# Optimization experiments

Hardware: AMD Instinct MI355X
Metric: run time of the kernel (lower is better)

## Reference

```python
import jax, jax.numpy as jnp
import numpy as np

EMB_DIM = 64
NUM_HEADS = 8
BATCH = 32
SEQ = 1024


def setup_inputs() -> dict:
    key = jax.random.key(0)
    k1, k2, k3 = jax.random.split(key, 3)
    hidden = EMB_DIM * NUM_HEADS  # 512
    x = jax.random.normal(k1, (BATCH, SEQ, EMB_DIM), dtype=jnp.float32)
    # torch Linear weights, stored here as (in, out) for x @ W
    w_qkv = jax.random.normal(k2, (EMB_DIM, 3 * hidden), dtype=jnp.float32) * (1.0 / np.sqrt(EMB_DIM))
    b_qkv = jnp.zeros((3 * hidden,), dtype=jnp.float32)
    w_proj = jax.random.normal(k3, (hidden, EMB_DIM), dtype=jnp.float32) * (1.0 / np.sqrt(hidden))
    b_proj = jnp.zeros((EMB_DIM,), dtype=jnp.float32)
    return {"x": x, "w_qkv": w_qkv, "b_qkv": b_qkv, "w_proj": w_proj, "b_proj": b_proj}


def reference(x, w_qkv, b_qkv, w_proj, b_proj):
    b, n, e = x.shape
    h = NUM_HEADS
    d = e  # per-head dim equals emb_dim in this module
    qkv = x @ w_qkv + b_qkv                      # (b, n, h*d*3), last axis layout (h, d, qkv)
    qkv = qkv.reshape(b, n, h, d, 3)
    qkv = jnp.transpose(qkv, (4, 0, 2, 1, 3))    # (3, b, h, n, d)
    q, k, v = qkv[0], qkv[1], qkv[2]
    energy = jnp.einsum('bhqd,bhkd->bhqk', q, k)  # (b, h, n, n)
    scale = jnp.asarray(e, dtype=x.dtype) ** 0.5  # `self.dim` in source; emb_dim is the intent
    attention = jax.nn.softmax(energy, axis=-1) / scale  # NOTE: divided AFTER softmax (faithful)
    # dropout p=0.0 -> identity
    out = jnp.einsum('bhal,bhlv->bhav', attention, v)    # (b, h, n, d)
    out = jnp.transpose(out, (0, 2, 1, 3)).reshape(b, n, h * d)
    return out @ w_proj + b_proj
```

## Files before the change

### kernel.cpp

```cpp
#include <hip/hip_runtime.h>
#include <hip/hip_bf16.h>

#define SEQ 1024
#define NH 8
#define HD 64
#define HID 512
#define BATCH 32
#define LOG2E 1.44269504f
#define KST 68

typedef _Float16 f16;
typedef f16 f16x4 __attribute__((ext_vector_type(4)));
typedef f16 f16x8 __attribute__((ext_vector_type(8)));
typedef float f32x4 __attribute__((ext_vector_type(4)));
typedef __fp16 h16x2 __attribute__((ext_vector_type(2)));

#define MFMA16 __builtin_amdgcn_mfma_f32_16x16x32_f16
#define EXP2F  __builtin_amdgcn_exp2f

__device__ __forceinline__ f16x8 ld8(const f16* p) {
    f16x4 a = *(const f16x4*)p;
    f16x4 b = *(const f16x4*)(p + 4);
    return __builtin_shufflevector(a, b, 0, 1, 2, 3, 4, 5, 6, 7);
}
__device__ __forceinline__ void st8(f16* p, f16x8 v) {
    *(f16x4*)p       = __builtin_shufflevector(v, v, 0, 1, 2, 3);
    *(f16x4*)(p + 4) = __builtin_shufflevector(v, v, 4, 5, 6, 7);
}

__global__ __launch_bounds__(256) void transpose_w(const float* __restrict__ wq,
                                                   const float* __restrict__ wp,
                                                   f16* __restrict__ wTq,
                                                   f16* __restrict__ wTp) {
    int flat = blockIdx.x * 256 + threadIdx.x;
    if (flat < 64 * 1536) {
        int e = flat / 1536, col = flat % 1536;
        int h = col / 192, r = col - h * 192;
        int d = r / 3, c = r - 3 * d;
        int jp = h * 192 + c * 64 + d;
        wTq[(size_t)jp * 64 + e] = (f16)wq[flat];
    } else {
        int f2 = flat - 64 * 1536;
        int k = f2 / 64, n = f2 % 64;
        wTp[(size_t)n * 512 + k] = (f16)wp[f2];
    }
}

__global__ __launch_bounds__(256) void qkv_kernel(const float* __restrict__ x,
                                                  const f16* __restrict__ wTq,
                                                  const float* __restrict__ b_qkv,
                                                  f16* __restrict__ Qb,
                                                  f16* __restrict__ Kb,
                                                  f16* __restrict__ Vtb) {
    __shared__ __align__(16) char smem[36864];
    f16* xs = (f16*)smem;
    f16* wsh = (f16*)(smem + 9216);
    f16* outs = (f16*)smem;

    const int n0   = blockIdx.x * 64;
    const int y    = blockIdx.y;
    const int b    = y & 31, h = y >> 5;
    const int bh   = b * NH + h;
    const int tid  = threadIdx.x;
    const int wave = tid >> 6, lane = tid & 63;
    const int quad = lane >> 4, l16 = lane & 15;

    for (int p = 0; p < 2; p++) {
        int t = tid + p * 256;
        int row = t >> 3, col = (t & 7) * 8;
        const float* src = x + ((size_t)(b * SEQ + n0 + row)) * 64 + col;
        float4 a0 = *(const float4*)src;
        float4 a1 = *(const float4*)(src + 4);
        f16x8 v = {(f16)a0.x, (f16)a0.y, (f16)a0.z, (f16)a0.w,
                   (f16)a1.x, (f16)a1.y, (f16)a1.z, (f16)a1.w};
        *(f16x8*)(&xs[row * 72 + col]) = v;
    }
    for (int p = 0; p < 6; p++) {
        int row = p * 32 + (tid >> 3), col = (tid & 7) * 8;
        *(f16x8*)(&wsh[row * 72 + col]) =
            *(const f16x8*)(wTq + (size_t)(h * 192 + row) * 64 + col);
    }
    __syncthreads();

    f16x8 af[2];
    af[0] = *(const f16x8*)(&xs[(wave * 16 + l16) * 72 + quad * 8]);
    af[1] = *(const f16x8*)(&xs[(wave * 16 + l16) * 72 + quad * 8 + 32]);

    f32x4 acc[12];
    f32x4 z = {0.f, 0.f, 0.f, 0.f};
    for (int jt = 0; jt < 12; jt++) acc[jt] = z;
    for (int jt = 0; jt < 12; jt++)
        for (int ss = 0; ss < 2; ss++) {
            f16x8 bf = *(const f16x8*)(&wsh[(jt * 16 + l16) * 72 + quad * 8 + ss * 32]);
            acc[jt] = MFMA16(af[ss], bf, acc[jt], 0, 0, 0);
        }

    __syncthreads();

    for (int jt = 0; jt < 12; jt++) {
        int c = jt >> 2, d = (jt & 3) * 16 + l16;
        float bias = b_qkv[h * 192 + d * 3 + c];
        float scl = (c == 0) ? LOG2E : 1.0f;
        for (int r = 0; r < 4; r++) {
            int nl = wave * 16 + quad * 4 + r;
            int off = (c < 2) ? (c * 4608 + nl * 72 + d) : (9216 + d * 72 + nl);
            outs[off] = (f16)((acc[jt][r] + bias) * scl);
        }
    }
    __syncthreads();

    {
        int rr = tid >> 2, ch = (tid & 3) * 16;
        f16x8 v0, v1;
        v0 = *(const f16x8*)(&outs[rr * 72 + ch]);
        v1 = *(const f16x8*)(&outs[rr * 72 + ch + 8]);
        f16* qd = Qb + ((size_t)bh * SEQ + n0 + rr) * HD + ch;
        *(f16x8*)qd = v0; *(f16x8*)(qd + 8) = v1;
        v0 = *(const f16x8*)(&outs[4608 + rr * 72 + ch]);
        v1 = *(const f16x8*)(&outs[4608 + rr * 72 + ch + 8]);
        f16* kd = Kb + ((size_t)bh * SEQ + n0 + rr) * HD + ch;
        *(f16x8*)kd = v0; *(f16x8*)(kd + 8) = v1;
        v0 = *(const f16x8*)(&outs[9216 + rr * 72 + ch]);
        v1 = *(const f16x8*)(&outs[9216 + rr * 72 + ch + 8]);
        f16* vd = Vtb + ((size_t)bh * HD + rr) * SEQ + n0 + ch;
        *(f16x8*)vd = v0; *(f16x8*)(vd + 8) = v1;
    }
}

__global__ __launch_bounds__(256, 4) void flash_kernel(const f16* __restrict__ Qb,
                                                       const f16* __restrict__ Kb,
                                                       const f16* __restrict__ Vtb,
                                                       f16* __restrict__ attn) {
    __shared__ __align__(16) f16 kv[2][2][64 * KST];

    const int id   = blockIdx.x;
    const int xcd  = id & 7;
    const int kk   = id >> 3;
    const int qt   = kk & 7;
    const int bh   = ((kk >> 3) << 3) | xcd;
    const int b    = bh >> 3, h = bh & 7;
    const int tid  = threadIdx.x;
    const int wave = tid >> 6, lane = tid & 63;
    const int quad = lane >> 4, l16 = lane & 15;

    const f16* kg = Kb  + (size_t)bh * SEQ * HD;
    const f16* vg = Vtb + (size_t)bh * HD * SEQ;

    const int region = wave >> 1;
    const int half   = wave & 1;
    const int lrow   = lane >> 3;
    const int lcol   = (lane & 7) * 8;

    {
        if (region == 0) {
            for (int p = 0; p < 4; p++) {
                int r = half * 32 + p * 8 + lrow;
                f16x8 v = *(const f16x8*)(kg + (size_t)r * HD + lcol);
                st8(&kv[0][0][r * KST + lcol], v);
            }
        } else {
            for (int p = 0; p < 4; p++) {
                int r = half * 32 + p * 8 + lrow;
                f16x8 v = *(const f16x8*)(vg + (size_t)r * SEQ + lcol);
                st8(&kv[0][1][r * KST + lcol], v);
            }
        }
    }

    const f16* Qp = Qb + ((size_t)bh * SEQ + qt * 128 + wave * 32) * HD;
    f16x8 qf[2][2];
    for (int j = 0; j < 2; j++)
        for (int ss = 0; ss < 2; ss++)
            qf[j][ss] = *(const f16x8*)(Qp + (size_t)(j * 16 + l16) * HD + ss * 32 + quad * 8);

    float m_st[2] = {-INFINITY, -INFINITY};
    float l_st[2] = {0.f, 0.f};
    f32x4 o[4][2];
    f32x4 z = {0.f, 0.f, 0.f, 0.f};
    for (int mt = 0; mt < 4; mt++) { o[mt][0] = z; o[mt][1] = z; }

    __syncthreads();

    for (int kt = 0; kt < SEQ / 64; kt++) {
        const int buf = kt & 1;

        f16x8 pf[4];
        if (kt < SEQ / 64 - 1) {
            if (region == 0) {
                const f16* g = kg + (size_t)((kt + 1) * 64) * HD;
                for (int p = 0; p < 4; p++) {
                    int r = half * 32 + p * 8 + lrow;
                    pf[p] = *(const f16x8*)(g + (size_t)r * HD + lcol);
                }
            } else {
                const f16* g = vg + (kt + 1) * 64;
                for (int p = 0; p < 4; p++) {
                    int r = half * 32 + p * 8 + lrow;
                    pf[p] = *(const f16x8*)(g + (size_t)r * SEQ + lcol);
                }
            }
        }

        const f16* ks = &kv[buf][0][0];
        const f16* vs = &kv[buf][1][0];
        f16* pw = &kv[buf ^ 1][0][0] + (wave * 2) * 16 * KST;

        f32x4 s[4][2];
        for (int ct = 0; ct < 4; ct++) {
            f16x8 ka = ld8(ks + (ct * 16 + l16) * KST + quad * 8);
            f16x8 kc = ld8(ks + (ct * 16 + l16) * KST + quad * 8 + 32);
            s[ct][0] = MFMA16(ka, qf[0][0], z, 0, 0, 0);
            s[ct][0] = MFMA16(kc, qf[0][1], s[ct][0], 0, 0, 0);
            s[ct][1] = MFMA16(ka, qf[1][0], z, 0, 0, 0);
            s[ct][1] = MFMA16(kc, qf[1][1], s[ct][1], 0, 0, 0);
        }

        for (int j = 0; j < 2; j++) {
            float mx = fmaxf(fmaxf(fmaxf(s[0][j][0], s[0][j][1]), fmaxf(s[0][j][2], s[0][j][3])),
                             fmaxf(fmaxf(s[1][j][0], s[1][j][1]), fmaxf(s[1][j][2], s[1][j][3])));
            mx = fmaxf(mx, fmaxf(fmaxf(fmaxf(s[2][j][0], s[2][j][1]), fmaxf(s[2][j][2], s[2][j][3])),
                                 fmaxf(fmaxf(s[3][j][0], s[3][j][1]), fmaxf(s[3][j][2], s[3][j][3]))));
            mx = fmaxf(mx, __shfl_xor(mx, 16, 64));
            mx = fmaxf(mx, __shfl_xor(mx, 32, 64));
            float mn = fmaxf(m_st[j], mx);
            float al = EXP2F(m_st[j] - mn);
            m_st[j] = mn;
            float rs = 0.f;
            for (int ct = 0; ct < 4; ct++)
                for (int r = 0; r < 4; r++) {
                    float p = EXP2F(s[ct][j][r] - mn);
                    s[ct][j][r] = p;
                    rs += p;
                }
            rs += __shfl_xor(rs, 16, 64);
            rs += __shfl_xor(rs, 32, 64);
            l_st[j] = l_st[j] * al + rs;
            if (!__all(al >= 1.0f))
                for (int mt = 0; mt < 4; mt++) o[mt][j] *= al;

            for (int ct = 0; ct < 4; ct++) {
                h16x2 lo = __builtin_amdgcn_cvt_pkrtz(s[ct][j][0], s[ct][j][1]);
                h16x2 hi = __builtin_amdgcn_cvt_pkrtz(s[ct][j][2], s[ct][j][3]);
                uint2 w = {__builtin_bit_cast(unsigned int, lo),
                           __builtin_bit_cast(unsigned int, hi)};
                *(uint2*)(pw + (j * 16 + l16) * KST + ct * 16 + quad * 4) = w;
            }
        }

        __asm__ volatile("s_waitcnt lgkmcnt(0)" ::: "memory");

        {
            f16x8 va[4];
            for (int mt = 0; mt < 4; mt++)
                va[mt] = ld8(vs + (mt * 16 + l16) * KST + quad * 8);
            f16x8 p0 = ld8(pw + l16 * KST + quad * 8);
            f16x8 p1 = ld8(pw + (16 + l16) * KST + quad * 8);
            for (int mt = 0; mt < 4; mt++) {
                o[mt][0] = MFMA16(va[mt], p0, o[mt][0], 0, 0, 0);
                o[mt][1] = MFMA16(va[mt], p1, o[mt][1], 0, 0, 0);
            }
            for (int mt = 0; mt < 4; mt++)
                va[mt] = ld8(vs + (mt * 16 + l16) * KST + quad * 8 + 32);
            p0 = ld8(pw + l16 * KST + quad * 8 + 32);
            p1 = ld8(pw + (16 + l16) * KST + quad * 8 + 32);
            for (int mt = 0; mt < 4; mt++) {
                o[mt][0] = MFMA16(va[mt], p0, o[mt][0], 0, 0, 0);
                o[mt][1] = MFMA16(va[mt], p1, o[mt][1], 0, 0, 0);
            }
        }

        if (kt < SEQ / 64 - 1) {
            f16* dst = &kv[buf ^ 1][region][0];
            for (int p = 0; p < 4; p++) {
                int r = half * 32 + p * 8 + lrow;
                st8(dst + r * KST + lcol, pf[p]);
            }
        }
        __syncthreads();
    }

    for (int j = 0; j < 2; j++) {
        float sc = 1.0f / (8.0f * l_st[j]);
        int n = qt * 128 + wave * 32 + j * 16 + l16;
        f16* op = attn + ((size_t)b * SEQ + n) * HID + h * HD + quad * 4;
        for (int mt = 0; mt < 4; mt++) {
            f16x4 w = {(f16)(o[mt][j][0] * sc), (f16)(o[mt][j][1] * sc),
                       (f16)(o[mt][j][2] * sc), (f16)(o[mt][j][3] * sc)};
            *(f16x4*)(op + mt * 16) = w;
        }
    }
}

__global__ __launch_bounds__(256) void proj_kernel(const f16* __restrict__ attn,
                                                   const f16* __restrict__ wTp,
                                                   const float* __restrict__ b_proj,
                                                   float* __restrict__ out) {
    __shared__ __align__(16) f16 a_lds[64][72];
    __shared__ __align__(16) f16 w_lds[64][72];

    const int blk  = blockIdx.x;
    const int tid  = threadIdx.x;
    const int wave = tid >> 6, lane = tid & 63;
    const int quad = lane >> 4, l16 = lane & 15;

    f32x4 acc[4];
    f32x4 z = {0.f, 0.f, 0.f, 0.f};
    for (int ct = 0; ct < 4; ct++) acc[ct] = z;

    for (int kt = 0; kt < 8; kt++) {
        __syncthreads();
        for (int p = 0; p < 2; p++) {
            int t = tid + p * 256;
            int row = t >> 3, col = (t & 7) * 8;
            *(f16x8*)(&a_lds[row][col]) =
                *(const f16x8*)(attn + ((size_t)(blk * 64 + row)) * HID + kt * 64 + col);
            *(f16x8*)(&w_lds[row][col]) =
                *(const f16x8*)(wTp + (size_t)row * HID + kt * 64 + col);
        }
        __syncthreads();
        for (int ss = 0; ss < 2; ss++) {
            f16x8 af = *(const f16x8*)(&a_lds[wave * 16 + l16][quad * 8 + ss * 32]);
            for (int ct = 0; ct < 4; ct++) {
                f16x8 bf = *(const f16x8*)(&w_lds[ct * 16 + l16][quad * 8 + ss * 32]);
                acc[ct] = MFMA16(af, bf, acc[ct], 0, 0, 0);
            }
        }
    }

    for (int ct = 0; ct < 4; ct++) {
        float bias = b_proj[ct * 16 + l16];
        for (int r = 0; r < 4; r++) {
            int row = blk * 64 + wave * 16 + quad * 4 + r;
            out[(size_t)row * HD + ct * 16 + l16] = acc[ct][r] + bias;
        }
    }
}

extern "C" void kernel_launch(void* const* d_in, const int* in_sizes, int n_in,
                              void* d_out, int out_size, void* d_ws, size_t ws_size,
                              hipStream_t stream) {
    (void)in_sizes; (void)n_in; (void)out_size; (void)ws_size;
    const float* x      = (const float*)d_in[0];
    const float* w_qkv  = (const float*)d_in[1];
    const float* b_qkv  = (const float*)d_in[2];
    const float* w_proj = (const float*)d_in[3];
    const float* b_proj = (const float*)d_in[4];
    float* out = (float*)d_out;

    char* ws = (char*)d_ws;
    const size_t QKV_EL = (size_t)BATCH * NH * SEQ * HD;
    f16* wTq  = (f16*)(ws);
    f16* wTp  = (f16*)(ws + 196608);
    f16* Qb   = (f16*)(ws + 262144);
    f16* Kb   = (f16*)(ws + 262144 + 2 * QKV_EL);
    f16* Vtb  = (f16*)(ws + 262144 + 4 * QKV_EL);
    f16* attn = (f16*)(ws + 262144 + 6 * QKV_EL);

    transpose_w<<<512, 256, 0, stream>>>(w_qkv, w_proj, wTq, wTp);
    qkv_kernel<<<dim3(16, BATCH * NH), 256, 0, stream>>>(x, wTq, b_qkv, Qb, Kb, Vtb);
    flash_kernel<<<2048, 256, 0, stream>>>(Qb, Kb, Vtb, attn);
    proj_kernel<<<512, 256, 0, stream>>>(attn, wTp, b_proj, out);
}
```

Measured before the change: 212.5 us.

## Compute softmax row sums via MFMA ones-row and double-buffer proj kernel

The flash kernel appends a row of ones to the V tile in shared memory, so the P·V MFMA also accumulates the softmax denominator. This removes the per-tile scalar row-sum reduction and its cross-lane shuffles, at the cost of extra MFMAs and more shared memory. Separately, the projection kernel now double-buffers its shared-memory tiles and prefetches the next K-slice into registers, dropping one barrier per iteration.

Result: faster. 206.6 us (-2.8%).

```diff
diff --git a/kernel.cpp b/kernel.cpp
--- a/kernel.cpp
+++ b/kernel.cpp
@@ -131,7 +131,8 @@
                                                        const f16* __restrict__ Kb,
                                                        const f16* __restrict__ Vtb,
                                                        f16* __restrict__ attn) {
-    __shared__ __align__(16) f16 kv[2][2][64 * KST];
+    __shared__ __align__(16) f16 kvk[2][64 * KST];
+    __shared__ __align__(16) f16 kvv[2][80 * KST];
 
     const int id   = blockIdx.x;
     const int xcd  = id & 7;
@@ -151,19 +152,22 @@
     const int lrow   = lane >> 3;
     const int lcol   = (lane & 7) * 8;
 
-    {
-        if (region == 0) {
-            for (int p = 0; p < 4; p++) {
-                int r = half * 32 + p * 8 + lrow;
-                f16x8 v = *(const f16x8*)(kg + (size_t)r * HD + lcol);
-                st8(&kv[0][0][r * KST + lcol], v);
-            }
-        } else {
-            for (int p = 0; p < 4; p++) {
-                int r = half * 32 + p * 8 + lrow;
-                f16x8 v = *(const f16x8*)(vg + (size_t)r * SEQ + lcol);
-                st8(&kv[0][1][r * KST + lcol], v);
-            }
+    if (tid < 128) {
+        int i = tid >> 6, c = tid & 63;
+        kvv[i][64 * KST + c] = (f16)1.0f;
+    }
+
+    if (region == 0) {
+        for (int p = 0; p < 4; p++) {
+            int r = half * 32 + p * 8 + lrow;
+            f16x8 v = *(const f16x8*)(kg + (size_t)r * HD + lcol);
+            st8(&kvk[0][r * KST + lcol], v);
+        }
+    } else {
+        for (int p = 0; p < 4; p++) {
+            int r = half * 32 + p * 8 + lrow;
+            f16x8 v = *(const f16x8*)(vg + (size_t)r * SEQ + lcol);
+            st8(&kvv[0][r * KST + lcol], v);
         }
     }
 
@@ -174,10 +178,9 @@
             qf[j][ss] = *(const f16x8*)(Qp + (size_t)(j * 16 + l16) * HD + ss * 32 + quad * 8);
 
     float m_st[2] = {-INFINITY, -INFINITY};
-    float l_st[2] = {0.f, 0.f};
-    f32x4 o[4][2];
+    f32x4 o[5][2];
     f32x4 z = {0.f, 0.f, 0.f, 0.f};
-    for (int mt = 0; mt < 4; mt++) { o[mt][0] = z; o[mt][1] = z; }
+    for (int mt = 0; mt < 5; mt++) { o[mt][0] = z; o[mt][1] = z; }
 
     __syncthreads();
 
@@ -201,9 +204,10 @@
             }
         }
 
-        const f16* ks = &kv[buf][0][0];
-        const f16* vs = &kv[buf][1][0];
-        f16* pw = &kv[buf ^ 1][0][0] + (wave * 2) * 16 * KST;
+        const f16* ks = &kvk[buf][0];
+        const f16* vs = &kvv[buf][0];
+        f16* pw = (wave < 2) ? &kvk[buf ^ 1][(wave & 1) * 32 * KST]
+                             : &kvv[buf ^ 1][(wave & 1) * 32 * KST];
 
         f32x4 s[4][2];
         for (int ct = 0; ct < 4; ct++) {
@@ -225,18 +229,11 @@
             float mn = fmaxf(m_st[j], mx);
             float al = EXP2F(m_st[j] - mn);
             m_st[j] = mn;
-            float rs = 0.f;
             for (int ct = 0; ct < 4; ct++)
-                for (int r = 0; r < 4; r++) {
-                    float p = EXP2F(s[ct][j][r] - mn);
-                    s[ct][j][r] = p;
-                    rs += p;
-                }
-            rs += __shfl_xor(rs, 16, 64);
-            rs += __shfl_xor(rs, 32, 64);
-            l_st[j] = l_st[j] * al + rs;
+                for (int r = 0; r < 4; r++)
+                    s[ct][j][r] = EXP2F(s[ct][j][r] - mn);
             if (!__all(al >= 1.0f))
-                for (int mt = 0; mt < 4; mt++) o[mt][j] *= al;
+                for (int mt = 0; mt < 5; mt++) o[mt][j] *= al;
 
             for (int ct = 0; ct < 4; ct++) {
                 h16x2 lo = __builtin_amdgcn_cvt_pkrtz(s[ct][j][0], s[ct][j][1]);
@@ -249,38 +246,38 @@
 
         __asm__ volatile("s_waitcnt lgkmcnt(0)" ::: "memory");
 
-        {
-            f16x8 va[4];
+        for (int c2 = 0; c2 < 2; c2++) {
+            f16x8 va[5];
             for (int mt = 0; mt < 4; mt++)
-                va[mt] = ld8(vs + (mt * 16 + l16) * KST + quad * 8);
-            f16x8 p0 = ld8(pw + l16 * KST + quad * 8);
-            f16x8 p1 = ld8(pw + (16 + l16) * KST + quad * 8);
-            for (int mt = 0; mt < 4; mt++) {
+                va[mt] = ld8(vs + (mt * 16 + l16) * KST + c2 * 32 + quad * 8);
+            va[4] = ld8(vs + (64 + l16) * KST + c2 * 32 + quad * 8);
+            f16x8 p0 = ld8(pw + l16 * KST + c2 * 32 + quad * 8);
+            f16x8 p1 = ld8(pw + (16 + l16) * KST + c2 * 32 + quad * 8);
+            for (int mt = 0; mt < 5; mt++) {
                 o[mt][0] = MFMA16(va[mt], p0, o[mt][0], 0, 0, 0);
                 o[mt][1] = MFMA16(va[mt], p1, o[mt][1], 0, 0, 0);
             }
-            for (int mt = 0; mt < 4; mt++)
-                va[mt] = ld8(vs + (mt * 16 + l16) * KST + quad * 8 + 32);
-            p0 = ld8(pw + l16 * KST + quad * 8 + 32);
-            p1 = ld8(pw + (16 + l16) * KST + quad * 8 + 32);
-            for (int mt = 0; mt < 4; mt++) {
-                o[mt][0] = MFMA16(va[mt], p0, o[mt][0], 0, 0, 0);
-                o[mt][1] = MFMA16(va[mt], p1, o[mt][1], 0, 0, 0);
-            }
         }
 
         if (kt < SEQ / 64 - 1) {
-            f16* dst = &kv[buf ^ 1][region][0];
-            for (int p = 0; p < 4; p++) {
-                int r = half * 32 + p * 8 + lrow;
-                st8(dst + r * KST + lcol, pf[p]);
+            if (region == 0) {
+                for (int p = 0; p < 4; p++) {
+                    int r = half * 32 + p * 8 + lrow;
+                    st8(&kvk[buf ^ 1][r * KST + lcol], pf[p]);
+                }
+            } else {
+                for (int p = 0; p < 4; p++) {
+                    int r = half * 32 + p * 8 + lrow;
+                    st8(&kvv[buf ^ 1][r * KST + lcol], pf[p]);
+                }
             }
         }
         __syncthreads();
     }
 
     for (int j = 0; j < 2; j++) {
-        float sc = 1.0f / (8.0f * l_st[j]);
+        float li = __shfl(o[4][j][0], l16, 64);
+        float sc = 1.0f / (8.0f * li);
         int n = qt * 128 + wave * 32 + j * 16 + l16;
         f16* op = attn + ((size_t)b * SEQ + n) * HID + h * HD + quad * 4;
         for (int mt = 0; mt < 4; mt++) {
@@ -295,33 +292,45 @@
                                                    const f16* __restrict__ wTp,
                                                    const float* __restrict__ b_proj,
                                                    float* __restrict__ out) {
-    __shared__ __align__(16) f16 a_lds[64][72];
-    __shared__ __align__(16) f16 w_lds[64][72];
+    __shared__ __align__(16) f16 a_lds[2][64 * 72];
+    __shared__ __align__(16) f16 w_lds[2][64 * 72];
 
     const int blk  = blockIdx.x;
     const int tid  = threadIdx.x;
     const int wave = tid >> 6, lane = tid & 63;
     const int quad = lane >> 4, l16 = lane & 15;
+    const int row0 = tid >> 3, col0 = (tid & 7) * 8;
+
+    const f16* ab = attn + (size_t)(blk * 64) * HID;
 
     f32x4 acc[4];
     f32x4 z = {0.f, 0.f, 0.f, 0.f};
     for (int ct = 0; ct < 4; ct++) acc[ct] = z;
 
+    f16x8 pa0 = *(const f16x8*)(ab + (size_t)row0 * HID + col0);
+    f16x8 pa1 = *(const f16x8*)(ab + (size_t)(row0 + 32) * HID + col0);
+    f16x8 pw0 = *(const f16x8*)(wTp + (size_t)row0 * HID + col0);
+    f16x8 pw1 = *(const f16x8*)(wTp + (size_t)(row0 + 32) * HID + col0);
+
     for (int kt = 0; kt < 8; kt++) {
+        const int buf = kt & 1;
+        *(f16x8*)(&a_lds[buf][row0 * 72 + col0])        = pa0;
+        *(f16x8*)(&a_lds[buf][(row0 + 32) * 72 + col0]) = pa1;
+        *(f16x8*)(&w_lds[buf][row0 * 72 + col0])        = pw0;
+        *(f16x8*)(&w_lds[buf][(row0 + 32) * 72 + col0]) = pw1;
         __syncthreads();
-        for (int p = 0; p < 2; p++) {
-            int t = tid + p * 256;
-            int row = t >> 3, col = (t & 7) * 8;
-            *(f16x8*)(&a_lds[row][col]) =
-                *(const f16x8*)(attn + ((size_t)(blk * 64 + row)) * HID + kt * 64 + col);
-            *(f16x8*)(&w_lds[row][col]) =
-                *(const f16x8*)(wTp + (size_t)row * HID + kt * 64 + col);
-        }
-        __syncthreads();
+
+        if (kt < 7) {
+            pa0 = *(const f16x8*)(ab + (size_t)row0 * HID + (kt + 1) * 64 + col0);
+            pa1 = *(const f16x8*)(ab + (size_t)(row0 + 32) * HID + (kt + 1) * 64 + col0);
+            pw0 = *(const f16x8*)(wTp + (size_t)row0 * HID + (kt + 1) * 64 + col0);
+            pw1 = *(const f16x8*)(wTp + (size_t)(row0 + 32) * HID + (kt + 1) * 64 + col0);
+        }
+
         for (int ss = 0; ss < 2; ss++) {
-            f16x8 af = *(const f16x8*)(&a_lds[wave * 16 + l16][quad * 8 + ss * 32]);
+            f16x8 af = *(const f16x8*)(&a_lds[buf][(wave * 16 + l16) * 72 + quad * 8 + ss * 32]);
             for (int ct = 0; ct < 4; ct++) {
-                f16x8 bf = *(const f16x8*)(&w_lds[ct * 16 + l16][quad * 8 + ss * 32]);
+                f16x8 bf = *(const f16x8*)(&w_lds[buf][(ct * 16 + l16) * 72 + quad * 8 + ss * 32]);
                 acc[ct] = MFMA16(af, bf, acc[ct], 0, 0, 0);
             }
         }
```

## Swizzle flash-attention LDS tiles and double-buffer projection kernel loads

Applied to the files above, without the earlier changes.

Replaces the padded (stride 68) K/V/P shared-memory tiles in the flash kernel with unpadded 64-wide rows using an XOR swizzle on 4-element chunks, so reads and writes avoid bank conflicts without padding. Separately, the projection GEMM now prefetches the next K-tile into registers and double-buffers LDS, dropping one barrier per iteration. The swizzle adds index arithmetic and keeps 8-byte split accesses. The single barrier per iteration relies on the two LDS buffers alternating, so correctness depends on that ordering.

Result: slower. 227.1 us (+6.9%).

```diff
diff --git a/kernel.cpp b/kernel.cpp
--- a/kernel.cpp
+++ b/kernel.cpp
@@ -7,7 +7,6 @@
 #define HID 512
 #define BATCH 32
 #define LOG2E 1.44269504f
-#define KST 68
 
 typedef _Float16 f16;
 typedef f16 f16x4 __attribute__((ext_vector_type(4)));
@@ -18,14 +17,8 @@
 #define MFMA16 __builtin_amdgcn_mfma_f32_16x16x32_f16
 #define EXP2F  __builtin_amdgcn_exp2f
 
-__device__ __forceinline__ f16x8 ld8(const f16* p) {
-    f16x4 a = *(const f16x4*)p;
-    f16x4 b = *(const f16x4*)(p + 4);
+__device__ __forceinline__ f16x8 cat44(f16x4 a, f16x4 b) {
     return __builtin_shufflevector(a, b, 0, 1, 2, 3, 4, 5, 6, 7);
-}
-__device__ __forceinline__ void st8(f16* p, f16x8 v) {
-    *(f16x4*)p       = __builtin_shufflevector(v, v, 0, 1, 2, 3);
-    *(f16x4*)(p + 4) = __builtin_shufflevector(v, v, 4, 5, 6, 7);
 }
 
 __global__ __launch_bounds__(256) void transpose_w(const float* __restrict__ wq,
@@ -131,7 +124,7 @@
                                                        const f16* __restrict__ Kb,
                                                        const f16* __restrict__ Vtb,
                                                        f16* __restrict__ attn) {
-    __shared__ __align__(16) f16 kv[2][2][64 * KST];
+    __shared__ __align__(16) f16 kv[2][2][64 * 64];
 
     const int id   = blockIdx.x;
     const int xcd  = id & 7;
@@ -150,20 +143,24 @@
     const int half   = wave & 1;
     const int lrow   = lane >> 3;
     const int lcol   = (lane & 7) * 8;
+    const int c0     = (lane & 7) * 2;
+    const int sAo0 = ((c0     ^ lrow) << 2), sAo1 = (((c0 + 1) ^ lrow) << 2);
+    const int sBo0 = ((c0 ^ (8 + lrow)) << 2), sBo1 = (((c0 + 1) ^ (8 + lrow)) << 2);
+
+    const int fA0 = ((2 * quad)     ^ l16) << 2, fA1 = ((2 * quad + 1) ^ l16) << 2;
+    const int fC0 = ((2 * quad + 8) ^ l16) << 2, fC1 = ((2 * quad + 9) ^ l16) << 2;
 
     {
-        if (region == 0) {
-            for (int p = 0; p < 4; p++) {
-                int r = half * 32 + p * 8 + lrow;
-                f16x8 v = *(const f16x8*)(kg + (size_t)r * HD + lcol);
-                st8(&kv[0][0][r * KST + lcol], v);
-            }
-        } else {
-            for (int p = 0; p < 4; p++) {
-                int r = half * 32 + p * 8 + lrow;
-                f16x8 v = *(const f16x8*)(vg + (size_t)r * SEQ + lcol);
-                st8(&kv[0][1][r * KST + lcol], v);
-            }
+        const f16* g = (region == 0) ? kg : vg;
+        const size_t gst = (region == 0) ? HD : SEQ;
+        f16* dst = &kv[0][region][0];
+        for (int p = 0; p < 4; p++) {
+            int r = half * 32 + p * 8 + lrow;
+            f16x8 v = *(const f16x8*)(g + (size_t)r * gst + lcol);
+            f16* rp = dst + r * 64;
+            int o0 = (p & 1) ? sBo0 : sAo0, o1 = (p & 1) ? sBo1 : sAo1;
+            *(f16x4*)(rp + o0) = __builtin_shufflevector(v, v, 0, 1, 2, 3);
+            *(f16x4*)(rp + o1) = __builtin_shufflevector(v, v, 4, 5, 6, 7);
         }
     }
 
@@ -179,6 +176,9 @@
     f32x4 z = {0.f, 0.f, 0.f, 0.f};
     for (int mt = 0; mt < 4; mt++) { o[mt][0] = z; o[mt][1] = z; }
 
+    int pwo[4];
+    for (int ct = 0; ct < 4; ct++) pwo[ct] = ((ct * 4 + quad) ^ l16) << 2;
+
     __syncthreads();
 
     for (int kt = 0; kt < SEQ / 64; kt++) {
@@ -186,29 +186,24 @@
 
         f16x8 pf[4];
         if (kt < SEQ / 64 - 1) {
-            if (region == 0) {
-                const f16* g = kg + (size_t)((kt + 1) * 64) * HD;
-                for (int p = 0; p < 4; p++) {
-                    int r = half * 32 + p * 8 + lrow;
-                    pf[p] = *(const f16x8*)(g + (size_t)r * HD + lcol);
-                }
-            } else {
-                const f16* g = vg + (kt + 1) * 64;
-                for (int p = 0; p < 4; p++) {
-                    int r = half * 32 + p * 8 + lrow;
-                    pf[p] = *(const f16x8*)(g + (size_t)r * SEQ + lcol);
-                }
+            const f16* g = (region == 0) ? (kg + (size_t)((kt + 1) * 64) * HD)
+                                         : (vg + (kt + 1) * 64);
+            const size_t gst = (region == 0) ? HD : SEQ;
+            for (int p = 0; p < 4; p++) {
+                int r = half * 32 + p * 8 + lrow;
+                pf[p] = *(const f16x8*)(g + (size_t)r * gst + lcol);
             }
         }
 
         const f16* ks = &kv[buf][0][0];
         const f16* vs = &kv[buf][1][0];
-        f16* pw = &kv[buf ^ 1][0][0] + (wave * 2) * 16 * KST;
+        f16* pw = &kv[buf ^ 1][wave >> 1][(wave & 1) * 32 * 64];
 
         f32x4 s[4][2];
         for (int ct = 0; ct < 4; ct++) {
-            f16x8 ka = ld8(ks + (ct * 16 + l16) * KST + quad * 8);
-            f16x8 kc = ld8(ks + (ct * 16 + l16) * KST + quad * 8 + 32);
+            const f16* kr = ks + (ct * 16 + l16) * 64;
+            f16x8 ka = cat44(*(const f16x4*)(kr + fA0), *(const f16x4*)(kr + fA1));
+            f16x8 kc = cat44(*(const f16x4*)(kr + fC0), *(const f16x4*)(kr + fC1));
             s[ct][0] = MFMA16(ka, qf[0][0], z, 0, 0, 0);
             s[ct][0] = MFMA16(kc, qf[0][1], s[ct][0], 0, 0, 0);
             s[ct][1] = MFMA16(ka, qf[1][0], z, 0, 0, 0);
@@ -238,31 +233,29 @@
             if (!__all(al >= 1.0f))
                 for (int mt = 0; mt < 4; mt++) o[mt][j] *= al;
 
+            f16* pr = pw + (j * 16 + l16) * 64;
             for (int ct = 0; ct < 4; ct++) {
                 h16x2 lo = __builtin_amdgcn_cvt_pkrtz(s[ct][j][0], s[ct][j][1]);
                 h16x2 hi = __builtin_amdgcn_cvt_pkrtz(s[ct][j][2], s[ct][j][3]);
                 uint2 w = {__builtin_bit_cast(unsigned int, lo),
                            __builtin_bit_cast(unsigned int, hi)};
-                *(uint2*)(pw + (j * 16 + l16) * KST + ct * 16 + quad * 4) = w;
+                *(uint2*)(pr + pwo[ct]) = w;
             }
         }
 
         __asm__ volatile("s_waitcnt lgkmcnt(0)" ::: "memory");
 
-        {
+        for (int c2 = 0; c2 < 2; c2++) {
+            const int o0 = c2 ? fC0 : fA0, o1 = c2 ? fC1 : fA1;
             f16x8 va[4];
-            for (int mt = 0; mt < 4; mt++)
-                va[mt] = ld8(vs + (mt * 16 + l16) * KST + quad * 8);
-            f16x8 p0 = ld8(pw + l16 * KST + quad * 8);
-            f16x8 p1 = ld8(pw + (16 + l16) * KST + quad * 8);
             for (int mt = 0; mt < 4; mt++) {
-                o[mt][0] = MFMA16(va[mt], p0, o[mt][0], 0, 0, 0);
-                o[mt][1] = MFMA16(va[mt], p1, o[mt][1], 0, 0, 0);
-            }
-            for (int mt = 0; mt < 4; mt++)
-                va[mt] = ld8(vs + (mt * 16 + l16) * KST + quad * 8 + 32);
-            p0 = ld8(pw + l16 * KST + quad * 8 + 32);
-            p1 = ld8(pw + (16 + l16) * KST + quad * 8 + 32);
+                const f16* vr = vs + (mt * 16 + l16) * 64;
+                va[mt] = cat44(*(const f16x4*)(vr + o0), *(const f16x4*)(vr + o1));
+            }
+            const f16* p0r = pw + l16 * 64;
+            const f16* p1r = pw + (16 + l16) * 64;
+            f16x8 p0 = cat44(*(const f16x4*)(p0r + o0), *(const f16x4*)(p0r + o1));
+            f16x8 p1 = cat44(*(const f16x4*)(p1r + o0), *(const f16x4*)(p1r + o1));
             for (int mt = 0; mt < 4; mt++) {
                 o[mt][0] = MFMA16(va[mt], p0, o[mt][0], 0, 0, 0);
                 o[mt][1] = MFMA16(va[mt], p1, o[mt][1], 0, 0, 0);
@@ -273,7 +266,10 @@
             f16* dst = &kv[buf ^ 1][region][0];
             for (int p = 0; p < 4; p++) {
                 int r = half * 32 + p * 8 + lrow;
-                st8(dst + r * KST + lcol, pf[p]);
+                f16* rp = dst + r * 64;
+                int o0 = (p & 1) ? sBo0 : sAo0, o1 = (p & 1) ? sBo1 : sAo1;
+                *(f16x4*)(rp + o0) = __builtin_shufflevector(pf[p], pf[p], 0, 1, 2, 3);
+                *(f16x4*)(rp + o1) = __builtin_shufflevector(pf[p], pf[p], 4, 5, 6, 7);
             }
         }
         __syncthreads();
@@ -295,33 +291,45 @@
                                                    const f16* __restrict__ wTp,
                                                    const float* __restrict__ b_proj,
                                                    float* __restrict__ out) {
-    __shared__ __align__(16) f16 a_lds[64][72];
-    __shared__ __align__(16) f16 w_lds[64][72];
+    __shared__ __align__(16) f16 a_lds[2][64 * 72];
+    __shared__ __align__(16) f16 w_lds[2][64 * 72];
 
     const int blk  = blockIdx.x;
     const int tid  = threadIdx.x;
     const int wave = tid >> 6, lane = tid & 63;
     const int quad = lane >> 4, l16 = lane & 15;
+    const int row0 = tid >> 3, col0 = (tid & 7) * 8;
+
+    const f16* ab = attn + (size_t)(blk * 64) * HID;
 
     f32x4 acc[4];
     f32x4 z = {0.f, 0.f, 0.f, 0.f};
     for (int ct = 0; ct < 4; ct++) acc[ct] = z;
 
+    f16x8 pa0 = *(const f16x8*)(ab + (size_t)row0 * HID + col0);
+    f16x8 pa1 = *(const f16x8*)(ab + (size_t)(row0 + 32) * HID + col0);
+    f16x8 pw0 = *(const f16x8*)(wTp + (size_t)row0 * HID + col0);
+    f16x8 pw1 = *(const f16x8*)(wTp + (size_t)(row0 + 32) * HID + col0);
+
     for (int kt = 0; kt < 8; kt++) {
+        const int buf = kt & 1;
+        *(f16x8*)(&a_lds[buf][row0 * 72 + col0])        = pa0;
+        *(f16x8*)(&a_lds[buf][(row0 + 32) * 72 + col0]) = pa1;
+        *(f16x8*)(&w_lds[buf][row0 * 72 + col0])        = pw0;
+        *(f16x8*)(&w_lds[buf][(row0 + 32) * 72 + col0]) = pw1;
         __syncthreads();
-        for (int p = 0; p < 2; p++) {
-            int t = tid + p * 256;
-            int row = t >> 3, col = (t & 7) * 8;
-            *(f16x8*)(&a_lds[row][col]) =
-                *(const f16x8*)(attn + ((size_t)(blk * 64 + row)) * HID + kt * 64 + col);
-            *(f16x8*)(&w_lds[row][col]) =
-                *(const f16x8*)(wTp + (size_t)row * HID + kt * 64 + col);
-        }
-        __syncthreads();
+
+        if (kt < 7) {
+            pa0 = *(const f16x8*)(ab + (size_t)row0 * HID + (kt + 1) * 64 + col0);
+            pa1 = *(const f16x8*)(ab + (size_t)(row0 + 32) * HID + (kt + 1) * 64 + col0);
+            pw0 = *(const f16x8*)(wTp + (size_t)row0 * HID + (kt + 1) * 64 + col0);
+            pw1 = *(const f16x8*)(wTp + (size_t)(row0 + 32) * HID + (kt + 1) * 64 + col0);
+        }
+
         for (int ss = 0; ss < 2; ss++) {
-            f16x8 af = *(const f16x8*)(&a_lds[wave * 16 + l16][quad * 8 + ss * 32]);
+            f16x8 af = *(const f16x8*)(&a_lds[buf][(wave * 16 + l16) * 72 + quad * 8 + ss * 32]);
             for (int ct = 0; ct < 4; ct++) {
-                f16x8 bf = *(const f16x8*)(&w_lds[ct * 16 + l16][quad * 8 + ss * 32]);
+                f16x8 bf = *(const f16x8*)(&w_lds[buf][(ct * 16 + l16) * 72 + quad * 8 + ss * 32]);
                 acc[ct] = MFMA16(af, bf, acc[ct], 0, 0, 0);
             }
         }
```
